# Performance work log

Measured on AMD Instinct MI355X. Metric: run time of the kernel, lower is better.

## Reference

```python
import jax, jax.numpy as jnp
import numpy as np

Q = 10000   # num_question
D = 64      # dim_s
M = 50      # size_m
B = 64      # batch
T = 512     # seq_len


def setup_inputs() -> dict:
    key = jax.random.key(0)
    ks = jax.random.split(key, 14)
    s = 1.0 / np.sqrt(D)
    inp = {
        "question": jax.random.randint(ks[0], (B, T), 0, Q, dtype=jnp.int32),
        "response": jax.random.randint(ks[1], (B, T), 0, 2, dtype=jnp.int32),
        "mask": jnp.ones((B, T), dtype=jnp.float32),
        "k_emb": jax.random.normal(ks[2], (Q, D), jnp.float32) * s,
        "v_emb": jax.random.normal(ks[3], (2 * Q, D), jnp.float32) * s,
        "Mk": jax.random.normal(ks[4], (M, D), jnp.float32) * np.sqrt(2.0 / D),
        "Mv0": jax.random.normal(ks[5], (M, D), jnp.float32) * np.sqrt(2.0 / D),
        "e_W": jax.random.normal(ks[6], (D, D), jnp.float32) * s,
        "e_b": jnp.zeros((D,), jnp.float32),
        "a_W": jax.random.normal(ks[7], (D, D), jnp.float32) * s,
        "a_b": jnp.zeros((D,), jnp.float32),
        "f_W": jax.random.normal(ks[8], (2 * D, D), jnp.float32) * (1.0 / np.sqrt(2 * D)),
        "f_b": jnp.zeros((D,), jnp.float32),
        "p_W": jax.random.normal(ks[9], (D, 1), jnp.float32) * s,
        "p_b": jnp.zeros((1,), jnp.float32),
    }
    return inp


def reference(question, response, mask, k_emb, v_emb, Mk, Mv0,
              e_W, e_b, a_W, a_b, f_W, f_b, p_W, p_b):
    num_q = k_emb.shape[0]
    bsz = question.shape[0]
    x = question + num_q * response                      # [B,T] combined ids
    k = k_emb[question]                                  # [B,T,D]
    v = v_emb[x]                                         # [B,T,D]
    w = jax.nn.softmax(k @ Mk.T, axis=-1)                # [B,T,M] read/write weights
    e = jax.nn.sigmoid(v @ e_W + e_b)                    # [B,T,D] erase
    a = jnp.tanh(v @ a_W + a_b)                          # [B,T,D] add

    def step(Mvt, inp):
        wt, et, at, mt = inp                             # [B,M],[B,D],[B,D],[B]
        Mvn = Mvt * (1.0 - wt[:, :, None] * et[:, None, :]) + wt[:, :, None] * at[:, None, :]
        Mvt = jnp.where(mt[:, None, None] == 1, Mvn, Mvt)
        return Mvt, Mvt

    Mv0b = jnp.broadcast_to(Mv0, (bsz,) + Mv0.shape)     # [B,M,D]
    xs = (jnp.swapaxes(w, 0, 1), jnp.swapaxes(e, 0, 1),
          jnp.swapaxes(a, 0, 1), mask.T)
    _, Mv_seq = jax.lax.scan(step, Mv0b, xs)             # [T,B,M,D] states after steps 0..T-1
    # read at step t (t>=1) uses state after step t-1
    Mv_read = jnp.swapaxes(Mv_seq[:-1], 0, 1)            # [B,T-1,M,D]
    read = jnp.einsum('btm,btmd->btd', w[:, 1:], Mv_read)
    f = jnp.tanh(jnp.concatenate([read, k[:, 1:]], axis=-1) @ f_W + f_b)
    p = (f @ p_W + p_b).squeeze(-1)                      # [B,T-1]
    return p
```

## Files before the change

kernel.cpp:

```cpp
#include <hip/hip_runtime.h>
#include <cstddef>

#define QN 10000
#define DD 64
#define MM 50
#define BB 64
#define TT 512
#define WPAD 52
#define MG 25

__global__ __launch_bounds__(256) void kPre(
    const int* __restrict__ question, const int* __restrict__ response,
    const float* __restrict__ mask,
    const float* __restrict__ k_emb, const float* __restrict__ v_emb,
    const float* __restrict__ Mk,
    const float* __restrict__ e_W, const float* __restrict__ e_b,
    const float* __restrict__ a_W, const float* __restrict__ a_b,
    float* __restrict__ w_buf, float* __restrict__ e_buf,
    float* __restrict__ a_buf) {
  const int lane = (int)(threadIdx.x & 63);
  const int wslot = __builtin_amdgcn_readfirstlane((int)(threadIdx.x >> 6));
  const int gw = blockIdx.x * 4 + wslot;
  const int NW = gridDim.x * 4;
  const int third = NW / 3;
  if (gw >= 3 * third) return;
  const int role = gw / third;
  const int idx = gw - role * third;
  const int stride4 = third * 4;

  if (role == 0) {
    float mk[64];
    const int mrow = lane < MM ? lane : (MM - 1);
#pragma unroll
    for (int i = 0; i < 64; i += 4) {
      const float4 t4 = *(const float4*)(Mk + mrow * 64 + i);
      mk[i] = t4.x; mk[i + 1] = t4.y; mk[i + 2] = t4.z; mk[i + 3] = t4.w;
    }
    for (int base = idx * 4; base < BB * TT; base += stride4) {
      const int4 q4 = *(const int4*)(question + base);
      const float* __restrict__ kr0 = k_emb + (size_t)q4.x * 64;
      const float* __restrict__ kr1 = k_emb + (size_t)q4.y * 64;
      const float* __restrict__ kr2 = k_emb + (size_t)q4.z * 64;
      const float* __restrict__ kr3 = k_emb + (size_t)q4.w * 64;
      float l00=0.f,l01=0.f,l02=0.f,l03=0.f;
      float l10=0.f,l11=0.f,l12=0.f,l13=0.f;
      float l20=0.f,l21=0.f,l22=0.f,l23=0.f;
      float l30=0.f,l31=0.f,l32=0.f,l33=0.f;
#pragma unroll
      for (int i = 0; i < 64; i += 4) {
        const float4 k0 = *(const float4*)(kr0 + i);
        const float4 k1 = *(const float4*)(kr1 + i);
        const float4 k2 = *(const float4*)(kr2 + i);
        const float4 k3 = *(const float4*)(kr3 + i);
        l00 = fmaf(k0.x, mk[i], l00); l01 = fmaf(k0.y, mk[i+1], l01);
        l02 = fmaf(k0.z, mk[i+2], l02); l03 = fmaf(k0.w, mk[i+3], l03);
        l10 = fmaf(k1.x, mk[i], l10); l11 = fmaf(k1.y, mk[i+1], l11);
        l12 = fmaf(k1.z, mk[i+2], l12); l13 = fmaf(k1.w, mk[i+3], l13);
        l20 = fmaf(k2.x, mk[i], l20); l21 = fmaf(k2.y, mk[i+1], l21);
        l22 = fmaf(k2.z, mk[i+2], l22); l23 = fmaf(k2.w, mk[i+3], l23);
        l30 = fmaf(k3.x, mk[i], l30); l31 = fmaf(k3.y, mk[i+1], l31);
        l32 = fmaf(k3.z, mk[i+2], l32); l33 = fmaf(k3.w, mk[i+3], l33);
      }
      float lm[4];
      lm[0] = (l00 + l01) + (l02 + l03);
      lm[1] = (l10 + l11) + (l12 + l13);
      lm[2] = (l20 + l21) + (l22 + l23);
      lm[3] = (l30 + l31) + (l32 + l33);
#pragma unroll
      for (int r = 0; r < 4; ++r) {
        float lv = (lane < MM) ? lm[r] : -3.4e38f;
#pragma unroll
        for (int off = 32; off > 0; off >>= 1) lv = fmaxf(lv, __shfl_xor(lv, off));
        float pe = (lane < MM) ? __expf(lm[r] - lv) : 0.f;
        float ss = pe;
#pragma unroll
        for (int off = 32; off > 0; off >>= 1) ss += __shfl_xor(ss, off);
        if (lane < MM) w_buf[(size_t)(base + r) * WPAD + lane] = pe / ss;
      }
    }
  } else if (role == 1) {
    float ew[64];
#pragma unroll
    for (int i = 0; i < 64; ++i) ew[i] = e_W[i * 64 + lane];
    const float eb = e_b[lane];
    for (int base = idx * 4; base < BB * TT; base += stride4) {
      const int4 q4 = *(const int4*)(question + base);
      const int4 r4 = *(const int4*)(response + base);
      const float4 m4 = *(const float4*)(mask + base);
      const float* __restrict__ v0 = v_emb + ((size_t)q4.x + (size_t)QN * r4.x) * 64;
      const float* __restrict__ v1 = v_emb + ((size_t)q4.y + (size_t)QN * r4.y) * 64;
      const float* __restrict__ v2 = v_emb + ((size_t)q4.z + (size_t)QN * r4.z) * 64;
      const float* __restrict__ v3 = v_emb + ((size_t)q4.w + (size_t)QN * r4.w) * 64;
      float e00 = eb, e01 = 0.f, e10 = eb, e11 = 0.f;
      float e20 = eb, e21 = 0.f, e30 = eb, e31 = 0.f;
#pragma unroll
      for (int i = 0; i < 64; i += 2) {
        const float2 a0 = *(const float2*)(v0 + i);
        const float2 a1 = *(const float2*)(v1 + i);
        const float2 a2 = *(const float2*)(v2 + i);
        const float2 a3 = *(const float2*)(v3 + i);
        e00 = fmaf(a0.x, ew[i], e00); e01 = fmaf(a0.y, ew[i+1], e01);
        e10 = fmaf(a1.x, ew[i], e10); e11 = fmaf(a1.y, ew[i+1], e11);
        e20 = fmaf(a2.x, ew[i], e20); e21 = fmaf(a2.y, ew[i+1], e21);
        e30 = fmaf(a3.x, ew[i], e30); e31 = fmaf(a3.y, ew[i+1], e31);
      }
      const float mf0 = (m4.x == 1.0f) ? 1.0f : 0.0f;
      const float mf1 = (m4.y == 1.0f) ? 1.0f : 0.0f;
      const float mf2 = (m4.z == 1.0f) ? 1.0f : 0.0f;
      const float mf3 = (m4.w == 1.0f) ? 1.0f : 0.0f;
      e_buf[(size_t)(base + 0) * 64 + lane] = mf0 / (1.f + __expf(-(e00 + e01)));
      e_buf[(size_t)(base + 1) * 64 + lane] = mf1 / (1.f + __expf(-(e10 + e11)));
      e_buf[(size_t)(base + 2) * 64 + lane] = mf2 / (1.f + __expf(-(e20 + e21)));
      e_buf[(size_t)(base + 3) * 64 + lane] = mf3 / (1.f + __expf(-(e30 + e31)));
    }
  } else {
    float aw[64];
#pragma unroll
    for (int i = 0; i < 64; ++i) aw[i] = a_W[i * 64 + lane];
    const float ab = a_b[lane];
    for (int base = idx * 4; base < BB * TT; base += stride4) {
      const int4 q4 = *(const int4*)(question + base);
      const int4 r4 = *(const int4*)(response + base);
      const float4 m4 = *(const float4*)(mask + base);
      const float* __restrict__ v0 = v_emb + ((size_t)q4.x + (size_t)QN * r4.x) * 64;
      const float* __restrict__ v1 = v_emb + ((size_t)q4.y + (size_t)QN * r4.y) * 64;
      const float* __restrict__ v2 = v_emb + ((size_t)q4.z + (size_t)QN * r4.z) * 64;
      const float* __restrict__ v3 = v_emb + ((size_t)q4.w + (size_t)QN * r4.w) * 64;
      float a00 = ab, a01 = 0.f, a10 = ab, a11 = 0.f;
      float a20 = ab, a21 = 0.f, a30 = ab, a31 = 0.f;
#pragma unroll
      for (int i = 0; i < 64; i += 2) {
        const float2 x0 = *(const float2*)(v0 + i);
        const float2 x1 = *(const float2*)(v1 + i);
        const float2 x2 = *(const float2*)(v2 + i);
        const float2 x3 = *(const float2*)(v3 + i);
        a00 = fmaf(x0.x, aw[i], a00); a01 = fmaf(x0.y, aw[i+1], a01);
        a10 = fmaf(x1.x, aw[i], a10); a11 = fmaf(x1.y, aw[i+1], a11);
        a20 = fmaf(x2.x, aw[i], a20); a21 = fmaf(x2.y, aw[i+1], a21);
        a30 = fmaf(x3.x, aw[i], a30); a31 = fmaf(x3.y, aw[i+1], a31);
      }
      const float mf0 = (m4.x == 1.0f) ? 1.0f : 0.0f;
      const float mf1 = (m4.y == 1.0f) ? 1.0f : 0.0f;
      const float mf2 = (m4.z == 1.0f) ? 1.0f : 0.0f;
      const float mf3 = (m4.w == 1.0f) ? 1.0f : 0.0f;
      const float s0 = a00 + a01, s1 = a10 + a11, s2 = a20 + a21, s3 = a30 + a31;
      a_buf[(size_t)(base + 0) * 64 + lane] = mf0 * (1.f - 2.f / (__expf(2.f * s0) + 1.f));
      a_buf[(size_t)(base + 1) * 64 + lane] = mf1 * (1.f - 2.f / (__expf(2.f * s1) + 1.f));
      a_buf[(size_t)(base + 2) * 64 + lane] = mf2 * (1.f - 2.f / (__expf(2.f * s2) + 1.f));
      a_buf[(size_t)(base + 3) * 64 + lane] = mf3 * (1.f - 2.f / (__expf(2.f * s3) + 1.f));
    }
  }
}

__global__ __launch_bounds__(256) void kA16(
    const float* __restrict__ w_buf, const float* __restrict__ e_buf,
    const float* __restrict__ a_buf, float* __restrict__ AB) {
  const int lane = (int)(threadIdx.x & 63);
  const int wslot = __builtin_amdgcn_readfirstlane((int)(threadIdx.x >> 6));
  const int u2 = blockIdx.x * 4 + wslot;
  if (u2 >= BB * 32 * 2) return;
  const int g = u2 & 1;
  const int unit = u2 >> 1;
  const int b = unit >> 5;
  const int c = unit & 31;
  const size_t rowbase = (size_t)b * TT + c * 16;
  const size_t eb0 = rowbase * 64 + lane;

  float ev[16], av[16];
#pragma unroll
  for (int j = 0; j < 16; ++j) {
    ev[j] = e_buf[eb0 + (size_t)j * 64];
    av[j] = a_buf[eb0 + (size_t)j * 64];
  }

  float Am[MG], Bm[MG];
#pragma unroll
  for (int m = 0; m < MG; ++m) { Am[m] = 1.f; Bm[m] = 0.f; }

#pragma unroll
  for (int j = 0; j < 16; ++j) {
    const float* __restrict__ wr = w_buf + (rowbase + j) * WPAD + g * MG;
#pragma unroll
    for (int m = 0; m < MG; ++m) {
      const float wm = wr[m];
      const float al = fmaf(-wm, ev[j], 1.0f);
      const float be = wm * av[j];
      Am[m] *= al;
      Bm[m] = fmaf(Bm[m], al, be);
    }
  }
  float* __restrict__ abp = AB + (size_t)unit * 6400 + (g * MG) * 128 + lane * 2;
#pragma unroll
  for (int m = 0; m < MG; ++m) {
    float2 o; o.x = Am[m]; o.y = Bm[m];
    *(float2*)(abp + m * 128) = o;
  }
}

__global__ __launch_bounds__(256) void kB_entry(
    const float* __restrict__ AB, const float* __restrict__ Mv0,
    float* __restrict__ entry, int C) {
  const int NT = gridDim.x * 256;
  for (int idx = blockIdx.x * 256 + (int)threadIdx.x; idx < BB * MM * 64;
       idx += NT) {
    const int b = idx / (MM * 64);
    const int r = idx - b * (MM * 64);
    float s = Mv0[r];
    const float* __restrict__ abp = AB + (size_t)b * C * 6400 + (size_t)r * 2;
    float* __restrict__ ep = entry + (size_t)b * C * 3200 + r;
    if (C == 32) {
      float2 ab[32];
#pragma unroll
      for (int c = 0; c < 32; ++c)
        ab[c] = *(const float2*)(abp + (size_t)c * 6400);
#pragma unroll
      for (int c = 0; c < 32; ++c) {
        ep[(size_t)c * 3200] = s;
        s = fmaf(ab[c].x, s, ab[c].y);
      }
    } else {
      float2 cur = *(const float2*)(abp);
      for (int c = 0; c < C; ++c) {
        ep[(size_t)c * 3200] = s;
        float2 nxt; nxt.x = 1.f; nxt.y = 0.f;
        if (c + 1 < C) nxt = *(const float2*)(abp + (size_t)(c + 1) * 6400);
        s = fmaf(cur.x, s, cur.y);
        cur = nxt;
      }
    }
  }
}

__global__ __launch_bounds__(256) void kC16(
    const float* __restrict__ w_buf, const float* __restrict__ e_buf,
    const float* __restrict__ a_buf, const float* __restrict__ entry,
    float* __restrict__ read2) {
  const int lane = (int)(threadIdx.x & 63);
  const int wslot = __builtin_amdgcn_readfirstlane((int)(threadIdx.x >> 6));
  const int u2 = blockIdx.x * 4 + wslot;
  if (u2 >= BB * 32 * 2) return;
  const int g = u2 & 1;
  const int unit = u2 >> 1;
  const int b = unit >> 5;
  const int c = unit & 31;
  const size_t RN = (size_t)BB * (TT - 1) * 64;
  const size_t rowbase = (size_t)b * TT + c * 16;
  const size_t eb0 = rowbase * 64 + lane;

  float ev[16], av[16];
#pragma unroll
  for (int j = 0; j < 16; ++j) {
    ev[j] = e_buf[eb0 + (size_t)j * 64];
    av[j] = a_buf[eb0 + (size_t)j * 64];
  }

  float s[MG];
  {
    const float* __restrict__ ep =
        entry + (size_t)unit * 3200 + (g * MG) * 64 + lane;
#pragma unroll
    for (int m = 0; m < MG; ++m) s[m] = ep[m * 64];
  }

  const int t0 = c * 16;
  float* __restrict__ rb = read2 + (size_t)g * RN;
#pragma unroll
  for (int j = 0; j < 16; ++j) {
    const int t = t0 + j;
    const float* __restrict__ wr = w_buf + (rowbase + j) * WPAD + g * MG;
    if (t >= 1) {
      float a0 = 0.f, a1 = 0.f;
#pragma unroll
      for (int m = 0; m < MG - 1; m += 2) {
        a0 = fmaf(wr[m], s[m], a0);
        a1 = fmaf(wr[m + 1], s[m + 1], a1);
      }
      a0 = fmaf(wr[MG - 1], s[MG - 1], a0);
      rb[((size_t)b * (TT - 1) + (t - 1)) * 64 + lane] = a0 + a1;
    }
#pragma unroll
    for (int m = 0; m < MG; ++m)
      s[m] = fmaf(wr[m], fmaf(-s[m], ev[j], av[j]), s[m]);
  }
}

__global__ __launch_bounds__(256) void kA_chunk(
    const float* __restrict__ w_buf, const float* __restrict__ e_buf,
    const float* __restrict__ a_buf, float* __restrict__ AB, int logC, int L) {
  const int lane = (int)(threadIdx.x & 63);
  const int wslot = __builtin_amdgcn_readfirstlane((int)(threadIdx.x >> 6));
  const int NW = gridDim.x * 4;
  const int C = 1 << logC;
  for (int u2 = blockIdx.x * 4 + wslot; u2 < BB * C * 2; u2 += NW) {
    const int g = u2 & 1;
    const int unit = u2 >> 1;
    const int b = unit >> logC;
    const int c = unit & (C - 1);
    float Am[MG], Bm[MG];
#pragma unroll
    for (int m = 0; m < MG; ++m) { Am[m] = 1.f; Bm[m] = 0.f; }
    const size_t rowbase = (size_t)b * TT + c * L;
#pragma unroll 2
    for (int j = 0; j < L; ++j) {
      const size_t row = rowbase + j;
      const float ed = e_buf[row * 64 + lane];
      const float ad = a_buf[row * 64 + lane];
      const float* __restrict__ wr = w_buf + row * WPAD + g * MG;
#pragma unroll
      for (int m = 0; m < MG; ++m) {
        const float wm = wr[m];
        const float al = fmaf(-wm, ed, 1.0f);
        const float be = wm * ad;
        Am[m] *= al;
        Bm[m] = fmaf(Bm[m], al, be);
      }
    }
    float* __restrict__ abp = AB + (size_t)unit * 6400 + (g * MG) * 128 + lane * 2;
#pragma unroll
    for (int m = 0; m < MG; ++m) {
      float2 o; o.x = Am[m]; o.y = Bm[m];
      *(float2*)(abp + m * 128) = o;
    }
  }
}

__global__ __launch_bounds__(256) void kC_read(
    const float* __restrict__ w_buf, const float* __restrict__ e_buf,
    const float* __restrict__ a_buf, const float* __restrict__ entry,
    const float* __restrict__ Mv0, float* __restrict__ read2,
    int logC, int L, int use_mv0) {
  const int lane = (int)(threadIdx.x & 63);
  const int wslot = __builtin_amdgcn_readfirstlane((int)(threadIdx.x >> 6));
  const int NW = gridDim.x * 4;
  const int C = 1 << logC;
  const size_t RN = (size_t)BB * (TT - 1) * 64;
  for (int u2 = blockIdx.x * 4 + wslot; u2 < BB * C * 2; u2 += NW) {
    const int g = u2 & 1;
    const int unit = u2 >> 1;
    const int b = unit >> logC;
    const int c = unit & (C - 1);
    float s[MG];
    if (use_mv0) {
#pragma unroll
      for (int m = 0; m < MG; ++m) s[m] = Mv0[(g * MG + m) * 64 + lane];
    } else {
      const float* __restrict__ ep =
          entry + (size_t)unit * 3200 + (g * MG) * 64 + lane;
#pragma unroll
      for (int m = 0; m < MG; ++m) s[m] = ep[m * 64];
    }
    const int t0 = c * L;
    float* __restrict__ rb = read2 + (size_t)g * RN;
    for (int j = 0; j < L; ++j) {
      const int t = t0 + j;
      const size_t row = (size_t)b * TT + t;
      const float ed = e_buf[row * 64 + lane];
      const float ad = a_buf[row * 64 + lane];
      const float* __restrict__ wr = w_buf + row * WPAD + g * MG;
      if (t >= 1) {
        float a0 = 0.f, a1 = 0.f;
#pragma unroll
        for (int m = 0; m < MG - 1; m += 2) {
          a0 = fmaf(wr[m], s[m], a0);
          a1 = fmaf(wr[m + 1], s[m + 1], a1);
        }
        a0 = fmaf(wr[MG - 1], s[MG - 1], a0);
        rb[((size_t)b * (TT - 1) + (t - 1)) * 64 + lane] = a0 + a1;
      }
#pragma unroll
      for (int m = 0; m < MG; ++m)
        s[m] = fmaf(wr[m], fmaf(-s[m], ed, ad), s[m]);
    }
  }
}

__global__ __launch_bounds__(256) void k3_out(
    const int* __restrict__ question, const float* __restrict__ k_emb,
    const float* __restrict__ read2,
    const float* __restrict__ f_W, const float* __restrict__ f_b,
    const float* __restrict__ p_W, const float* __restrict__ p_b,
    float* __restrict__ out) {
  const int lane = (int)(threadIdx.x & 63);
  const int wslot = __builtin_amdgcn_readfirstlane((int)(threadIdx.x >> 6));
  const int NW = gridDim.x * 4;
  const size_t RN = (size_t)BB * (TT - 1) * 64;

  float fw[128];
#pragma unroll
  for (int i = 0; i < 128; ++i) fw[i] = f_W[i * 64 + lane];
  const float fb = f_b[lane];
  const float pw = p_W[lane];
  const float pb = p_b[0];

  for (int row = blockIdx.x * 4 + wslot; row < BB * (TT - 1); row += NW) {
    const int b = row / (TT - 1);
    const int tp = row - b * (TT - 1);
    const float* __restrict__ r0 = read2 + (size_t)row * 64;
    const float* __restrict__ r1 = r0 + RN;
    const int qn = question[b * TT + tp + 1];
    const float* __restrict__ krow = k_emb + (size_t)qn * 64;

    float f0 = fb, f1 = 0.f, f2 = 0.f, f3 = 0.f;
#pragma unroll
    for (int i = 0; i < 64; i += 4) {
      const float4 x0 = *(const float4*)(r0 + i);
      const float4 x1 = *(const float4*)(r1 + i);
      f0 = fmaf(x0.x + x1.x, fw[i], f0);
      f1 = fmaf(x0.y + x1.y, fw[i + 1], f1);
      f2 = fmaf(x0.z + x1.z, fw[i + 2], f2);
      f3 = fmaf(x0.w + x1.w, fw[i + 3], f3);
    }
#pragma unroll
    for (int i = 0; i < 64; i += 4) {
      const float4 kv = *(const float4*)(krow + i);
      f0 = fmaf(kv.x, fw[64 + i], f0);
      f1 = fmaf(kv.y, fw[64 + i + 1], f1);
      f2 = fmaf(kv.z, fw[64 + i + 2], f2);
      f3 = fmaf(kv.w, fw[64 + i + 3], f3);
    }
    const float f = (f0 + f1) + (f2 + f3);
    const float t2 = __expf(2.f * f);
    const float fv = 1.f - 2.f / (t2 + 1.f);
    float acc = fv * pw;
#pragma unroll
    for (int off = 32; off > 0; off >>= 1) acc += __shfl_xor(acc, off);
    if (lane == 0) out[row] = acc + pb;
  }
}

extern "C" void kernel_launch(void* const* d_in, const int* in_sizes, int n_in,
                              void* d_out, int out_size, void* d_ws, size_t ws_size,
                              hipStream_t stream) {
  const int*   question = (const int*)d_in[0];
  const int*   response = (const int*)d_in[1];
  const float* mask     = (const float*)d_in[2];
  const float* k_emb    = (const float*)d_in[3];
  const float* v_emb    = (const float*)d_in[4];
  const float* Mk       = (const float*)d_in[5];
  const float* Mv0      = (const float*)d_in[6];
  const float* e_W      = (const float*)d_in[7];
  const float* e_b      = (const float*)d_in[8];
  const float* a_W      = (const float*)d_in[9];
  const float* a_b      = (const float*)d_in[10];
  const float* f_W      = (const float*)d_in[11];
  const float* f_b      = (const float*)d_in[12];
  const float* p_W      = (const float*)d_in[13];
  const float* p_b      = (const float*)d_in[14];
  float* out = (float*)d_out;

  const size_t wN  = (size_t)BB * TT * WPAD;
  const size_t eN  = (size_t)BB * TT * 64;
  const size_t r2N = 2ull * BB * (TT - 1) * 64;
  float* ws = (float*)d_ws;
  float* w_buf  = ws;
  float* e_buf  = w_buf + wN;
  float* a_buf  = e_buf + eN;
  float* read2  = a_buf + eN;
  float* AB_arr = read2 + r2N;
  const size_t baseN = wN + 2 * eN + r2N;

  int C = 32, logC = 5;
  while (C >= 2) {
    const size_t need = (baseN + 9600ull * BB * C) * sizeof(float);
    if (need <= ws_size) break;
    C >>= 1; logC -= 1;
  }
  int useChunks = (C >= 2);
  if (!useChunks) { C = 1; logC = 0; }
  const int L = TT / C;
  float* entry = AB_arr + 6400ull * BB * C;

  hipLaunchKernelGGL(kPre, dim3(2048), dim3(256), 0, stream,
                     question, response, mask, k_emb, v_emb, Mk,
                     e_W, e_b, a_W, a_b, w_buf, e_buf, a_buf);

  if (C == 32) {
    hipLaunchKernelGGL(kA16, dim3(1024), dim3(256), 0, stream,
                       w_buf, e_buf, a_buf, AB_arr);
    hipLaunchKernelGGL(kB_entry, dim3((BB * MM * 64 + 255) / 256), dim3(256),
                       0, stream, AB_arr, Mv0, entry, C);
    hipLaunchKernelGGL(kC16, dim3(1024), dim3(256), 0, stream,
                       w_buf, e_buf, a_buf, entry, read2);
  } else {
    if (useChunks) {
      const int ublocksA = (BB * C * 2 + 3) / 4;
      hipLaunchKernelGGL(kA_chunk, dim3(ublocksA), dim3(256), 0, stream,
                         w_buf, e_buf, a_buf, AB_arr, logC, L);
      hipLaunchKernelGGL(kB_entry, dim3((BB * MM * 64 + 255) / 256), dim3(256),
                         0, stream, AB_arr, Mv0, entry, C);
    }
    const int ublocksC = (BB * C * 2 + 3) / 4;
    hipLaunchKernelGGL(kC_read, dim3(ublocksC), dim3(256), 0, stream,
                       w_buf, e_buf, a_buf, entry, Mv0, read2,
                       logC, L, useChunks ? 0 : 1);
  }

  hipLaunchKernelGGL(k3_out, dim3(1024), dim3(256), 0, stream,
                     question, k_emb, read2, f_W, f_b, p_W, p_b, out);
}
```

Baseline: 211.4 us.

## Stage gathered embedding rows through LDS and prefetch next row in output kernel

In the precompute and output kernels, each lane now loads one element of each gathered embedding or read row with a coalesced load and writes it to a per-wave LDS buffer. The dot products then read broadcast float4 values from LDS instead of every lane issuing redundant wide global loads of the same row. The output kernel also software-prefetches the next row's read and key data. Empty asm constraints pin the weight arrays in VGPRs to stop the compiler rematerializing them. The LDS round trip relies on wave-synchronous execution with no barrier, and the pinning raises register pressure.

After: 225.6 us. +6.7%, slower.

```diff
diff --git a/kernel.cpp b/kernel.cpp
--- a/kernel.cpp
+++ b/kernel.cpp
@@ -8,6 +8,10 @@
 #define TT 512
 #define WPAD 52
 #define MG 25
+
+#define PIN(arr, n)                                        \
+  _Pragma("unroll") for (int _p = 0; _p < (n); ++_p)       \
+      asm volatile("" : "+v"((arr)[_p]));
 
 __global__ __launch_bounds__(256) void kPre(
     const int* __restrict__ question, const int* __restrict__ response,
@@ -18,9 +22,10 @@
     const float* __restrict__ a_W, const float* __restrict__ a_b,
     float* __restrict__ w_buf, float* __restrict__ e_buf,
     float* __restrict__ a_buf) {
+  __shared__ float stg[4][4][64];
   const int lane = (int)(threadIdx.x & 63);
-  const int wslot = __builtin_amdgcn_readfirstlane((int)(threadIdx.x >> 6));
-  const int gw = blockIdx.x * 4 + wslot;
+  const int ws = __builtin_amdgcn_readfirstlane((int)(threadIdx.x >> 6));
+  const int gw = blockIdx.x * 4 + ws;
   const int NW = gridDim.x * 4;
   const int third = NW / 3;
   if (gw >= 3 * third) return;
@@ -36,36 +41,31 @@
       const float4 t4 = *(const float4*)(Mk + mrow * 64 + i);
       mk[i] = t4.x; mk[i + 1] = t4.y; mk[i + 2] = t4.z; mk[i + 3] = t4.w;
     }
+    PIN(mk, 64)
     for (int base = idx * 4; base < BB * TT; base += stride4) {
       const int4 q4 = *(const int4*)(question + base);
-      const float* __restrict__ kr0 = k_emb + (size_t)q4.x * 64;
-      const float* __restrict__ kr1 = k_emb + (size_t)q4.y * 64;
-      const float* __restrict__ kr2 = k_emb + (size_t)q4.z * 64;
-      const float* __restrict__ kr3 = k_emb + (size_t)q4.w * 64;
-      float l00=0.f,l01=0.f,l02=0.f,l03=0.f;
-      float l10=0.f,l11=0.f,l12=0.f,l13=0.f;
-      float l20=0.f,l21=0.f,l22=0.f,l23=0.f;
-      float l30=0.f,l31=0.f,l32=0.f,l33=0.f;
-#pragma unroll
-      for (int i = 0; i < 64; i += 4) {
-        const float4 k0 = *(const float4*)(kr0 + i);
-        const float4 k1 = *(const float4*)(kr1 + i);
-        const float4 k2 = *(const float4*)(kr2 + i);
-        const float4 k3 = *(const float4*)(kr3 + i);
-        l00 = fmaf(k0.x, mk[i], l00); l01 = fmaf(k0.y, mk[i+1], l01);
-        l02 = fmaf(k0.z, mk[i+2], l02); l03 = fmaf(k0.w, mk[i+3], l03);
-        l10 = fmaf(k1.x, mk[i], l10); l11 = fmaf(k1.y, mk[i+1], l11);
-        l12 = fmaf(k1.z, mk[i+2], l12); l13 = fmaf(k1.w, mk[i+3], l13);
-        l20 = fmaf(k2.x, mk[i], l20); l21 = fmaf(k2.y, mk[i+1], l21);
-        l22 = fmaf(k2.z, mk[i+2], l22); l23 = fmaf(k2.w, mk[i+3], l23);
-        l30 = fmaf(k3.x, mk[i], l30); l31 = fmaf(k3.y, mk[i+1], l31);
-        l32 = fmaf(k3.z, mk[i+2], l32); l33 = fmaf(k3.w, mk[i+3], l33);
-      }
+      const float kl0 = k_emb[(size_t)q4.x * 64 + lane];
+      const float kl1 = k_emb[(size_t)q4.y * 64 + lane];
+      const float kl2 = k_emb[(size_t)q4.z * 64 + lane];
+      const float kl3 = k_emb[(size_t)q4.w * 64 + lane];
+      stg[ws][0][lane] = kl0;
+      stg[ws][1][lane] = kl1;
+      stg[ws][2][lane] = kl2;
+      stg[ws][3][lane] = kl3;
       float lm[4];
-      lm[0] = (l00 + l01) + (l02 + l03);
-      lm[1] = (l10 + l11) + (l12 + l13);
-      lm[2] = (l20 + l21) + (l22 + l23);
-      lm[3] = (l30 + l31) + (l32 + l33);
+#pragma unroll
+      for (int r = 0; r < 4; ++r) {
+        float l0 = 0.f, l1 = 0.f, l2 = 0.f, l3 = 0.f;
+#pragma unroll
+        for (int i = 0; i < 64; i += 4) {
+          const float4 kv = *(const float4*)&stg[ws][r][i];
+          l0 = fmaf(kv.x, mk[i], l0);
+          l1 = fmaf(kv.y, mk[i + 1], l1);
+          l2 = fmaf(kv.z, mk[i + 2], l2);
+          l3 = fmaf(kv.w, mk[i + 3], l3);
+        }
+        lm[r] = (l0 + l1) + (l2 + l3);
+      }
 #pragma unroll
       for (int r = 0; r < 4; ++r) {
         float lv = (lane < MM) ? lm[r] : -3.4e38f;
@@ -82,27 +82,36 @@
     float ew[64];
 #pragma unroll
     for (int i = 0; i < 64; ++i) ew[i] = e_W[i * 64 + lane];
+    PIN(ew, 64)
     const float eb = e_b[lane];
     for (int base = idx * 4; base < BB * TT; base += stride4) {
       const int4 q4 = *(const int4*)(question + base);
       const int4 r4 = *(const int4*)(response + base);
       const float4 m4 = *(const float4*)(mask + base);
-      const float* __restrict__ v0 = v_emb + ((size_t)q4.x + (size_t)QN * r4.x) * 64;
-      const float* __restrict__ v1 = v_emb + ((size_t)q4.y + (size_t)QN * r4.y) * 64;
-      const float* __restrict__ v2 = v_emb + ((size_t)q4.z + (size_t)QN * r4.z) * 64;
-      const float* __restrict__ v3 = v_emb + ((size_t)q4.w + (size_t)QN * r4.w) * 64;
+      const float vl0 = v_emb[((size_t)q4.x + (size_t)QN * r4.x) * 64 + lane];
+      const float vl1 = v_emb[((size_t)q4.y + (size_t)QN * r4.y) * 64 + lane];
+      const float vl2 = v_emb[((size_t)q4.z + (size_t)QN * r4.z) * 64 + lane];
+      const float vl3 = v_emb[((size_t)q4.w + (size_t)QN * r4.w) * 64 + lane];
+      stg[ws][0][lane] = vl0;
+      stg[ws][1][lane] = vl1;
+      stg[ws][2][lane] = vl2;
+      stg[ws][3][lane] = vl3;
       float e00 = eb, e01 = 0.f, e10 = eb, e11 = 0.f;
       float e20 = eb, e21 = 0.f, e30 = eb, e31 = 0.f;
 #pragma unroll
-      for (int i = 0; i < 64; i += 2) {
-        const float2 a0 = *(const float2*)(v0 + i);
-        const float2 a1 = *(const float2*)(v1 + i);
-        const float2 a2 = *(const float2*)(v2 + i);
-        const float2 a3 = *(const float2*)(v3 + i);
-        e00 = fmaf(a0.x, ew[i], e00); e01 = fmaf(a0.y, ew[i+1], e01);
-        e10 = fmaf(a1.x, ew[i], e10); e11 = fmaf(a1.y, ew[i+1], e11);
-        e20 = fmaf(a2.x, ew[i], e20); e21 = fmaf(a2.y, ew[i+1], e21);
-        e30 = fmaf(a3.x, ew[i], e30); e31 = fmaf(a3.y, ew[i+1], e31);
+      for (int i = 0; i < 64; i += 4) {
+        const float4 v0 = *(const float4*)&stg[ws][0][i];
+        const float4 v1 = *(const float4*)&stg[ws][1][i];
+        const float4 v2 = *(const float4*)&stg[ws][2][i];
+        const float4 v3 = *(const float4*)&stg[ws][3][i];
+        e00 = fmaf(v0.x, ew[i], e00);     e01 = fmaf(v0.y, ew[i + 1], e01);
+        e00 = fmaf(v0.z, ew[i + 2], e00); e01 = fmaf(v0.w, ew[i + 3], e01);
+        e10 = fmaf(v1.x, ew[i], e10);     e11 = fmaf(v1.y, ew[i + 1], e11);
+        e10 = fmaf(v1.z, ew[i + 2], e10); e11 = fmaf(v1.w, ew[i + 3], e11);
+        e20 = fmaf(v2.x, ew[i], e20);     e21 = fmaf(v2.y, ew[i + 1], e21);
+        e20 = fmaf(v2.z, ew[i + 2], e20); e21 = fmaf(v2.w, ew[i + 3], e21);
+        e30 = fmaf(v3.x, ew[i], e30);     e31 = fmaf(v3.y, ew[i + 1], e31);
+        e30 = fmaf(v3.z, ew[i + 2], e30); e31 = fmaf(v3.w, ew[i + 3], e31);
       }
       const float mf0 = (m4.x == 1.0f) ? 1.0f : 0.0f;
       const float mf1 = (m4.y == 1.0f) ? 1.0f : 0.0f;
@@ -117,27 +126,36 @@
     float aw[64];
 #pragma unroll
     for (int i = 0; i < 64; ++i) aw[i] = a_W[i * 64 + lane];
+    PIN(aw, 64)
     const float ab = a_b[lane];
     for (int base = idx * 4; base < BB * TT; base += stride4) {
       const int4 q4 = *(const int4*)(question + base);
       const int4 r4 = *(const int4*)(response + base);
       const float4 m4 = *(const float4*)(mask + base);
-      const float* __restrict__ v0 = v_emb + ((size_t)q4.x + (size_t)QN * r4.x) * 64;
-      const float* __restrict__ v1 = v_emb + ((size_t)q4.y + (size_t)QN * r4.y) * 64;
-      const float* __restrict__ v2 = v_emb + ((size_t)q4.z + (size_t)QN * r4.z) * 64;
-      const float* __restrict__ v3 = v_emb + ((size_t)q4.w + (size_t)QN * r4.w) * 64;
+      const float vl0 = v_emb[((size_t)q4.x + (size_t)QN * r4.x) * 64 + lane];
+      const float vl1 = v_emb[((size_t)q4.y + (size_t)QN * r4.y) * 64 + lane];
+      const float vl2 = v_emb[((size_t)q4.z + (size_t)QN * r4.z) * 64 + lane];
+      const float vl3 = v_emb[((size_t)q4.w + (size_t)QN * r4.w) * 64 + lane];
+      stg[ws][0][lane] = vl0;
+      stg[ws][1][lane] = vl1;
+      stg[ws][2][lane] = vl2;
+      stg[ws][3][lane] = vl3;
       float a00 = ab, a01 = 0.f, a10 = ab, a11 = 0.f;
       float a20 = ab, a21 = 0.f, a30 = ab, a31 = 0.f;
 #pragma unroll
-      for (int i = 0; i < 64; i += 2) {
-        const float2 x0 = *(const float2*)(v0 + i);
-        const float2 x1 = *(const float2*)(v1 + i);
-        const float2 x2 = *(const float2*)(v2 + i);
-        const float2 x3 = *(const float2*)(v3 + i);
-        a00 = fmaf(x0.x, aw[i], a00); a01 = fmaf(x0.y, aw[i+1], a01);
-        a10 = fmaf(x1.x, aw[i], a10); a11 = fmaf(x1.y, aw[i+1], a11);
-        a20 = fmaf(x2.x, aw[i], a20); a21 = fmaf(x2.y, aw[i+1], a21);
-        a30 = fmaf(x3.x, aw[i], a30); a31 = fmaf(x3.y, aw[i+1], a31);
+      for (int i = 0; i < 64; i += 4) {
+        const float4 v0 = *(const float4*)&stg[ws][0][i];
+        const float4 v1 = *(const float4*)&stg[ws][1][i];
+        const float4 v2 = *(const float4*)&stg[ws][2][i];
+        const float4 v3 = *(const float4*)&stg[ws][3][i];
+        a00 = fmaf(v0.x, aw[i], a00);     a01 = fmaf(v0.y, aw[i + 1], a01);
+        a00 = fmaf(v0.z, aw[i + 2], a00); a01 = fmaf(v0.w, aw[i + 3], a01);
+        a10 = fmaf(v1.x, aw[i], a10);     a11 = fmaf(v1.y, aw[i + 1], a11);
+        a10 = fmaf(v1.z, aw[i + 2], a10); a11 = fmaf(v1.w, aw[i + 3], a11);
+        a20 = fmaf(v2.x, aw[i], a20);     a21 = fmaf(v2.y, aw[i + 1], a21);
+        a20 = fmaf(v2.z, aw[i + 2], a20); a21 = fmaf(v2.w, aw[i + 3], a21);
+        a30 = fmaf(v3.x, aw[i], a30);     a31 = fmaf(v3.y, aw[i + 1], a31);
+        a30 = fmaf(v3.z, aw[i + 2], a30); a31 = fmaf(v3.w, aw[i + 3], a31);
       }
       const float mf0 = (m4.x == 1.0f) ? 1.0f : 0.0f;
       const float mf1 = (m4.y == 1.0f) ? 1.0f : 0.0f;
@@ -380,39 +398,55 @@
     const float* __restrict__ f_W, const float* __restrict__ f_b,
     const float* __restrict__ p_W, const float* __restrict__ p_b,
     float* __restrict__ out) {
+  __shared__ float stg[4][2][64];
   const int lane = (int)(threadIdx.x & 63);
-  const int wslot = __builtin_amdgcn_readfirstlane((int)(threadIdx.x >> 6));
+  const int ws = __builtin_amdgcn_readfirstlane((int)(threadIdx.x >> 6));
   const int NW = gridDim.x * 4;
   const size_t RN = (size_t)BB * (TT - 1) * 64;
+  const int R = BB * (TT - 1);
 
   float fw[128];
 #pragma unroll
   for (int i = 0; i < 128; ++i) fw[i] = f_W[i * 64 + lane];
+  PIN(fw, 128)
   const float fb = f_b[lane];
   const float pw = p_W[lane];
   const float pb = p_b[0];
 
-  for (int row = blockIdx.x * 4 + wslot; row < BB * (TT - 1); row += NW) {
+  int row = blockIdx.x * 4 + ws;
+  float rd = 0.f, kl = 0.f;
+  if (row < R) {
+    rd = read2[(size_t)row * 64 + lane] + read2[RN + (size_t)row * 64 + lane];
     const int b = row / (TT - 1);
     const int tp = row - b * (TT - 1);
-    const float* __restrict__ r0 = read2 + (size_t)row * 64;
-    const float* __restrict__ r1 = r0 + RN;
     const int qn = question[b * TT + tp + 1];
-    const float* __restrict__ krow = k_emb + (size_t)qn * 64;
-
+    kl = k_emb[(size_t)qn * 64 + lane];
+  }
+  while (row < R) {
+    const int nrow = row + NW;
+    float nrd = 0.f, nkl = 0.f;
+    if (nrow < R) {
+      nrd = read2[(size_t)nrow * 64 + lane] +
+            read2[RN + (size_t)nrow * 64 + lane];
+      const int nb = nrow / (TT - 1);
+      const int ntp = nrow - nb * (TT - 1);
+      const int nqn = question[nb * TT + ntp + 1];
+      nkl = k_emb[(size_t)nqn * 64 + lane];
+    }
+    stg[ws][0][lane] = rd;
+    stg[ws][1][lane] = kl;
     float f0 = fb, f1 = 0.f, f2 = 0.f, f3 = 0.f;
 #pragma unroll
     for (int i = 0; i < 64; i += 4) {
-      const float4 x0 = *(const float4*)(r0 + i);
-      const float4 x1 = *(const float4*)(r1 + i);
-      f0 = fmaf(x0.x + x1.x, fw[i], f0);
-      f1 = fmaf(x0.y + x1.y, fw[i + 1], f1);
-      f2 = fmaf(x0.z + x1.z, fw[i + 2], f2);
-      f3 = fmaf(x0.w + x1.w, fw[i + 3], f3);
+      const float4 xv = *(const float4*)&stg[ws][0][i];
+      f0 = fmaf(xv.x, fw[i], f0);
+      f1 = fmaf(xv.y, fw[i + 1], f1);
+      f2 = fmaf(xv.z, fw[i + 2], f2);
+      f3 = fmaf(xv.w, fw[i + 3], f3);
     }
 #pragma unroll
     for (int i = 0; i < 64; i += 4) {
-      const float4 kv = *(const float4*)(krow + i);
+      const float4 kv = *(const float4*)&stg[ws][1][i];
       f0 = fmaf(kv.x, fw[64 + i], f0);
       f1 = fmaf(kv.y, fw[64 + i + 1], f1);
       f2 = fmaf(kv.z, fw[64 + i + 2], f2);
@@ -425,6 +459,8 @@
 #pragma unroll
     for (int off = 32; off > 0; off >>= 1) acc += __shfl_xor(acc, off);
     if (lane == 0) out[row] = acc + pb;
+
+    rd = nrd; kl = nkl; row = nrow;
   }
 }
 
```

## Replace chunked parallel scan with single-pass per-batch sequential scan kernel

Applied to the files above, without the earlier changes.

Drops the three-phase chunked scan (chunk transfer coefficients, entry-state propagation, re-scan with reads). In its place is one kernel per batch row: four compute waves each own a slice of the memory rows, producer waves double-buffer e/a/w into LDS, and a writer wave reduces the partial reads into a single read buffer. This removes the AB and entry intermediate traffic, two kernel launches and the duplicated scan work. The cost is a fully serial 512-step loop on only 64 blocks, which leaves most of the GPU idle and adds a block barrier every chunk. The output kernel is also changed to prefetch the next row, stage it through LDS and pin the weight registers.

Result: slower. 310.7 us (+46.9%).

```diff
diff --git a/kernel.cpp b/kernel.cpp
--- a/kernel.cpp
+++ b/kernel.cpp
@@ -7,7 +7,10 @@
 #define BB 64
 #define TT 512
 #define WPAD 52
-#define MG 25
+
+#define PIN(arr, n)                                        \
+  _Pragma("unroll") for (int _p = 0; _p < (n); ++_p)       \
+      asm volatile("" : "+v"((arr)[_p]));
 
 __global__ __launch_bounds__(256) void kPre(
     const int* __restrict__ question, const int* __restrict__ response,
@@ -152,267 +155,181 @@
   }
 }
 
-__global__ __launch_bounds__(256) void kA16(
+__global__ __launch_bounds__(512) void kScan(
     const float* __restrict__ w_buf, const float* __restrict__ e_buf,
-    const float* __restrict__ a_buf, float* __restrict__ AB) {
+    const float* __restrict__ a_buf, const float* __restrict__ Mv0,
+    float* __restrict__ read_buf) {
+  __shared__ float e_lds[2][16][64];
+  __shared__ float a_lds[2][16][64];
+  __shared__ float w_lds[2][4][16][16];
+  __shared__ float p_lds[2][4][16][64];
   const int lane = (int)(threadIdx.x & 63);
-  const int wslot = __builtin_amdgcn_readfirstlane((int)(threadIdx.x >> 6));
-  const int u2 = blockIdx.x * 4 + wslot;
-  if (u2 >= BB * 32 * 2) return;
-  const int g = u2 & 1;
-  const int unit = u2 >> 1;
-  const int b = unit >> 5;
-  const int c = unit & 31;
-  const size_t rowbase = (size_t)b * TT + c * 16;
-  const size_t eb0 = rowbase * 64 + lane;
-
-  float ev[16], av[16];
-#pragma unroll
-  for (int j = 0; j < 16; ++j) {
-    ev[j] = e_buf[eb0 + (size_t)j * 64];
-    av[j] = a_buf[eb0 + (size_t)j * 64];
-  }
-
-  float Am[MG], Bm[MG];
-#pragma unroll
-  for (int m = 0; m < MG; ++m) { Am[m] = 1.f; Bm[m] = 0.f; }
-
-#pragma unroll
-  for (int j = 0; j < 16; ++j) {
-    const float* __restrict__ wr = w_buf + (rowbase + j) * WPAD + g * MG;
-#pragma unroll
-    for (int m = 0; m < MG; ++m) {
-      const float wm = wr[m];
-      const float al = fmaf(-wm, ev[j], 1.0f);
-      const float be = wm * av[j];
-      Am[m] *= al;
-      Bm[m] = fmaf(Bm[m], al, be);
-    }
-  }
-  float* __restrict__ abp = AB + (size_t)unit * 6400 + (g * MG) * 128 + lane * 2;
-#pragma unroll
-  for (int m = 0; m < MG; ++m) {
-    float2 o; o.x = Am[m]; o.y = Bm[m];
-    *(float2*)(abp + m * 128) = o;
-  }
-}
-
-__global__ __launch_bounds__(256) void kB_entry(
-    const float* __restrict__ AB, const float* __restrict__ Mv0,
-    float* __restrict__ entry, int C) {
-  const int NT = gridDim.x * 256;
-  for (int idx = blockIdx.x * 256 + (int)threadIdx.x; idx < BB * MM * 64;
-       idx += NT) {
-    const int b = idx / (MM * 64);
-    const int r = idx - b * (MM * 64);
-    float s = Mv0[r];
-    const float* __restrict__ abp = AB + (size_t)b * C * 6400 + (size_t)r * 2;
-    float* __restrict__ ep = entry + (size_t)b * C * 3200 + r;
-    if (C == 32) {
-      float2 ab[32];
-#pragma unroll
-      for (int c = 0; c < 32; ++c)
-        ab[c] = *(const float2*)(abp + (size_t)c * 6400);
-#pragma unroll
-      for (int c = 0; c < 32; ++c) {
-        ep[(size_t)c * 3200] = s;
-        s = fmaf(ab[c].x, s, ab[c].y);
+  const int ws = __builtin_amdgcn_readfirstlane((int)(threadIdx.x >> 6));
+  const int b = blockIdx.x;
+  const size_t bbase = (size_t)b * TT;
+
+  float s[13];
+  if (ws < 4) {
+    const int gbase = (ws < 2) ? ws * 13 : 26 + (ws - 2) * 12;
+    const int gcnt  = (ws < 2) ? 13 : 12;
+#pragma unroll
+    for (int m = 0; m < 13; ++m)
+      s[m] = (m < gcnt) ? Mv0[(gbase + m) * 64 + lane] : 0.f;
+  }
+
+  if (ws == 4) {
+#pragma unroll
+    for (int j = 0; j < 16; ++j)
+      e_lds[0][j][lane] = e_buf[(bbase + j) * 64 + lane];
+  } else if (ws == 5) {
+#pragma unroll
+    for (int j = 0; j < 16; ++j)
+      a_lds[0][j][lane] = a_buf[(bbase + j) * 64 + lane];
+  } else if (ws == 6) {
+#pragma unroll
+    for (int j = 0; j < 16; ++j) {
+      if (lane < MM) {
+        const float v = w_buf[(bbase + j) * WPAD + lane];
+        const int grp = (lane < 13) ? 0 : (lane < 26) ? 1 : (lane < 38) ? 2 : 3;
+        const int gb = (grp < 2) ? grp * 13 : 26 + (grp - 2) * 12;
+        w_lds[0][grp][j][lane - gb] = v;
+      } else if (lane == 50) w_lds[0][2][j][12] = 0.f;
+      else if (lane == 51) w_lds[0][3][j][12] = 0.f;
+    }
+  }
+  __syncthreads();
+
+  for (int c = 0; c < 32; ++c) {
+    const int p = c & 1;
+    if (ws < 4) {
+      const int g = ws;
+#pragma unroll
+      for (int j = 0; j < 16; ++j) {
+        const float4 q0 = *(const float4*)&w_lds[p][g][j][0];
+        const float4 q1 = *(const float4*)&w_lds[p][g][j][4];
+        const float4 q2 = *(const float4*)&w_lds[p][g][j][8];
+        const float4 q3 = *(const float4*)&w_lds[p][g][j][12];
+        const float ed = e_lds[p][j][lane];
+        const float ad = a_lds[p][j][lane];
+        const float wm[13] = {q0.x, q0.y, q0.z, q0.w, q1.x, q1.y, q1.z, q1.w,
+                              q2.x, q2.y, q2.z, q2.w, q3.x};
+        float d0 = 0.f, d1 = 0.f;
+#pragma unroll
+        for (int m = 0; m < 12; m += 2) {
+          d0 = fmaf(wm[m], s[m], d0);
+          d1 = fmaf(wm[m + 1], s[m + 1], d1);
+        }
+        d0 = fmaf(wm[12], s[12], d0);
+        p_lds[p][g][j][lane] = d0 + d1;
+#pragma unroll
+        for (int m = 0; m < 13; ++m)
+          s[m] = fmaf(wm[m], fmaf(-s[m], ed, ad), s[m]);
+      }
+    } else if (ws == 4) {
+      if (c + 1 < 32) {
+        const size_t rb = bbase + (size_t)(c + 1) * 16;
+#pragma unroll
+        for (int j = 0; j < 16; ++j)
+          e_lds[1 - p][j][lane] = e_buf[(rb + j) * 64 + lane];
+      }
+    } else if (ws == 5) {
+      if (c + 1 < 32) {
+        const size_t rb = bbase + (size_t)(c + 1) * 16;
+#pragma unroll
+        for (int j = 0; j < 16; ++j)
+          a_lds[1 - p][j][lane] = a_buf[(rb + j) * 64 + lane];
+      }
+    } else if (ws == 6) {
+      if (c + 1 < 32) {
+        const size_t rb = bbase + (size_t)(c + 1) * 16;
+#pragma unroll
+        for (int j = 0; j < 16; ++j) {
+          if (lane < MM) {
+            const float v = w_buf[(rb + j) * WPAD + lane];
+            const int grp = (lane < 13) ? 0 : (lane < 26) ? 1 : (lane < 38) ? 2 : 3;
+            const int gb = (grp < 2) ? grp * 13 : 26 + (grp - 2) * 12;
+            w_lds[1 - p][grp][j][lane - gb] = v;
+          } else if (lane == 50) w_lds[1 - p][2][j][12] = 0.f;
+          else if (lane == 51) w_lds[1 - p][3][j][12] = 0.f;
+        }
       }
     } else {
-      float2 cur = *(const float2*)(abp);
-      for (int c = 0; c < C; ++c) {
-        ep[(size_t)c * 3200] = s;
-        float2 nxt; nxt.x = 1.f; nxt.y = 0.f;
-        if (c + 1 < C) nxt = *(const float2*)(abp + (size_t)(c + 1) * 6400);
-        s = fmaf(cur.x, s, cur.y);
-        cur = nxt;
-      }
-    }
-  }
-}
-
-__global__ __launch_bounds__(256) void kC16(
-    const float* __restrict__ w_buf, const float* __restrict__ e_buf,
-    const float* __restrict__ a_buf, const float* __restrict__ entry,
-    float* __restrict__ read2) {
-  const int lane = (int)(threadIdx.x & 63);
-  const int wslot = __builtin_amdgcn_readfirstlane((int)(threadIdx.x >> 6));
-  const int u2 = blockIdx.x * 4 + wslot;
-  if (u2 >= BB * 32 * 2) return;
-  const int g = u2 & 1;
-  const int unit = u2 >> 1;
-  const int b = unit >> 5;
-  const int c = unit & 31;
-  const size_t RN = (size_t)BB * (TT - 1) * 64;
-  const size_t rowbase = (size_t)b * TT + c * 16;
-  const size_t eb0 = rowbase * 64 + lane;
-
-  float ev[16], av[16];
-#pragma unroll
-  for (int j = 0; j < 16; ++j) {
-    ev[j] = e_buf[eb0 + (size_t)j * 64];
-    av[j] = a_buf[eb0 + (size_t)j * 64];
-  }
-
-  float s[MG];
-  {
-    const float* __restrict__ ep =
-        entry + (size_t)unit * 3200 + (g * MG) * 64 + lane;
-#pragma unroll
-    for (int m = 0; m < MG; ++m) s[m] = ep[m * 64];
-  }
-
-  const int t0 = c * 16;
-  float* __restrict__ rb = read2 + (size_t)g * RN;
-#pragma unroll
-  for (int j = 0; j < 16; ++j) {
-    const int t = t0 + j;
-    const float* __restrict__ wr = w_buf + (rowbase + j) * WPAD + g * MG;
-    if (t >= 1) {
-      float a0 = 0.f, a1 = 0.f;
-#pragma unroll
-      for (int m = 0; m < MG - 1; m += 2) {
-        a0 = fmaf(wr[m], s[m], a0);
-        a1 = fmaf(wr[m + 1], s[m + 1], a1);
-      }
-      a0 = fmaf(wr[MG - 1], s[MG - 1], a0);
-      rb[((size_t)b * (TT - 1) + (t - 1)) * 64 + lane] = a0 + a1;
-    }
-#pragma unroll
-    for (int m = 0; m < MG; ++m)
-      s[m] = fmaf(wr[m], fmaf(-s[m], ev[j], av[j]), s[m]);
-  }
-}
-
-__global__ __launch_bounds__(256) void kA_chunk(
-    const float* __restrict__ w_buf, const float* __restrict__ e_buf,
-    const float* __restrict__ a_buf, float* __restrict__ AB, int logC, int L) {
-  const int lane = (int)(threadIdx.x & 63);
-  const int wslot = __builtin_amdgcn_readfirstlane((int)(threadIdx.x >> 6));
-  const int NW = gridDim.x * 4;
-  const int C = 1 << logC;
-  for (int u2 = blockIdx.x * 4 + wslot; u2 < BB * C * 2; u2 += NW) {
-    const int g = u2 & 1;
-    const int unit = u2 >> 1;
-    const int b = unit >> logC;
-    const int c = unit & (C - 1);
-    float Am[MG], Bm[MG];
-#pragma unroll
-    for (int m = 0; m < MG; ++m) { Am[m] = 1.f; Bm[m] = 0.f; }
-    const size_t rowbase = (size_t)b * TT + c * L;
-#pragma unroll 2
-    for (int j = 0; j < L; ++j) {
-      const size_t row = rowbase + j;
-      const float ed = e_buf[row * 64 + lane];
-      const float ad = a_buf[row * 64 + lane];
-      const float* __restrict__ wr = w_buf + row * WPAD + g * MG;
-#pragma unroll
-      for (int m = 0; m < MG; ++m) {
-        const float wm = wr[m];
-        const float al = fmaf(-wm, ed, 1.0f);
-        const float be = wm * ad;
-        Am[m] *= al;
-        Bm[m] = fmaf(Bm[m], al, be);
-      }
-    }
-    float* __restrict__ abp = AB + (size_t)unit * 6400 + (g * MG) * 128 + lane * 2;
-#pragma unroll
-    for (int m = 0; m < MG; ++m) {
-      float2 o; o.x = Am[m]; o.y = Bm[m];
-      *(float2*)(abp + m * 128) = o;
-    }
-  }
-}
-
-__global__ __launch_bounds__(256) void kC_read(
-    const float* __restrict__ w_buf, const float* __restrict__ e_buf,
-    const float* __restrict__ a_buf, const float* __restrict__ entry,
-    const float* __restrict__ Mv0, float* __restrict__ read2,
-    int logC, int L, int use_mv0) {
-  const int lane = (int)(threadIdx.x & 63);
-  const int wslot = __builtin_amdgcn_readfirstlane((int)(threadIdx.x >> 6));
-  const int NW = gridDim.x * 4;
-  const int C = 1 << logC;
-  const size_t RN = (size_t)BB * (TT - 1) * 64;
-  for (int u2 = blockIdx.x * 4 + wslot; u2 < BB * C * 2; u2 += NW) {
-    const int g = u2 & 1;
-    const int unit = u2 >> 1;
-    const int b = unit >> logC;
-    const int c = unit & (C - 1);
-    float s[MG];
-    if (use_mv0) {
-#pragma unroll
-      for (int m = 0; m < MG; ++m) s[m] = Mv0[(g * MG + m) * 64 + lane];
-    } else {
-      const float* __restrict__ ep =
-          entry + (size_t)unit * 3200 + (g * MG) * 64 + lane;
-#pragma unroll
-      for (int m = 0; m < MG; ++m) s[m] = ep[m * 64];
-    }
-    const int t0 = c * L;
-    float* __restrict__ rb = read2 + (size_t)g * RN;
-    for (int j = 0; j < L; ++j) {
-      const int t = t0 + j;
-      const size_t row = (size_t)b * TT + t;
-      const float ed = e_buf[row * 64 + lane];
-      const float ad = a_buf[row * 64 + lane];
-      const float* __restrict__ wr = w_buf + row * WPAD + g * MG;
-      if (t >= 1) {
-        float a0 = 0.f, a1 = 0.f;
-#pragma unroll
-        for (int m = 0; m < MG - 1; m += 2) {
-          a0 = fmaf(wr[m], s[m], a0);
-          a1 = fmaf(wr[m + 1], s[m + 1], a1);
+      if (c >= 1) {
+        const int cc = c - 1, q = 1 - p;
+        const int j0 = (cc == 0) ? 1 : 0;
+        for (int j = j0; j < 16; ++j) {
+          const int t = cc * 16 + j;
+          const float r = (p_lds[q][0][j][lane] + p_lds[q][1][j][lane]) +
+                          (p_lds[q][2][j][lane] + p_lds[q][3][j][lane]);
+          read_buf[((size_t)b * (TT - 1) + (t - 1)) * 64 + lane] = r;
         }
-        a0 = fmaf(wr[MG - 1], s[MG - 1], a0);
-        rb[((size_t)b * (TT - 1) + (t - 1)) * 64 + lane] = a0 + a1;
-      }
-#pragma unroll
-      for (int m = 0; m < MG; ++m)
-        s[m] = fmaf(wr[m], fmaf(-s[m], ed, ad), s[m]);
+      }
+    }
+    __syncthreads();
+  }
+  if (ws == 7) {
+    for (int j = 0; j < 16; ++j) {
+      const int t = 31 * 16 + j;
+      const float r = (p_lds[1][0][j][lane] + p_lds[1][1][j][lane]) +
+                      (p_lds[1][2][j][lane] + p_lds[1][3][j][lane]);
+      read_buf[((size_t)b * (TT - 1) + (t - 1)) * 64 + lane] = r;
     }
   }
 }
 
 __global__ __launch_bounds__(256) void k3_out(
     const int* __restrict__ question, const float* __restrict__ k_emb,
-    const float* __restrict__ read2,
+    const float* __restrict__ read_buf,
     const float* __restrict__ f_W, const float* __restrict__ f_b,
     const float* __restrict__ p_W, const float* __restrict__ p_b,
     float* __restrict__ out) {
+  __shared__ float stg[4][2][64];
   const int lane = (int)(threadIdx.x & 63);
-  const int wslot = __builtin_amdgcn_readfirstlane((int)(threadIdx.x >> 6));
+  const int ws = __builtin_amdgcn_readfirstlane((int)(threadIdx.x >> 6));
   const int NW = gridDim.x * 4;
-  const size_t RN = (size_t)BB * (TT - 1) * 64;
+  const int R = BB * (TT - 1);
 
   float fw[128];
 #pragma unroll
   for (int i = 0; i < 128; ++i) fw[i] = f_W[i * 64 + lane];
+  PIN(fw, 128)
   const float fb = f_b[lane];
   const float pw = p_W[lane];
   const float pb = p_b[0];
 
-  for (int row = blockIdx.x * 4 + wslot; row < BB * (TT - 1); row += NW) {
+  int row = blockIdx.x * 4 + ws;
+  float rd = 0.f, kl = 0.f;
+  if (row < R) {
+    rd = read_buf[(size_t)row * 64 + lane];
     const int b = row / (TT - 1);
     const int tp = row - b * (TT - 1);
-    const float* __restrict__ r0 = read2 + (size_t)row * 64;
-    const float* __restrict__ r1 = r0 + RN;
     const int qn = question[b * TT + tp + 1];
-    const float* __restrict__ krow = k_emb + (size_t)qn * 64;
-
+    kl = k_emb[(size_t)qn * 64 + lane];
+  }
+  while (row < R) {
+    const int nrow = row + NW;
+    float nrd = 0.f, nkl = 0.f;
+    if (nrow < R) {
+      nrd = read_buf[(size_t)nrow * 64 + lane];
+      const int nb = nrow / (TT - 1);
+      const int ntp = nrow - nb * (TT - 1);
+      const int nqn = question[nb * TT + ntp + 1];
+      nkl = k_emb[(size_t)nqn * 64 + lane];
+    }
+    stg[ws][0][lane] = rd;
+    stg[ws][1][lane] = kl;
     float f0 = fb, f1 = 0.f, f2 = 0.f, f3 = 0.f;
 #pragma unroll
     for (int i = 0; i < 64; i += 4) {
-      const float4 x0 = *(const float4*)(r0 + i);
-      const float4 x1 = *(const float4*)(r1 + i);
-      f0 = fmaf(x0.x + x1.x, fw[i], f0);
-      f1 = fmaf(x0.y + x1.y, fw[i + 1], f1);
-      f2 = fmaf(x0.z + x1.z, fw[i + 2], f2);
-      f3 = fmaf(x0.w + x1.w, fw[i + 3], f3);
+      const float4 xv = *(const float4*)&stg[ws][0][i];
+      f0 = fmaf(xv.x, fw[i], f0);
+      f1 = fmaf(xv.y, fw[i + 1], f1);
+      f2 = fmaf(xv.z, fw[i + 2], f2);
+      f3 = fmaf(xv.w, fw[i + 3], f3);
     }
 #pragma unroll
     for (int i = 0; i < 64; i += 4) {
-      const float4 kv = *(const float4*)(krow + i);
+      const float4 kv = *(const float4*)&stg[ws][1][i];
       f0 = fmaf(kv.x, fw[64 + i], f0);
       f1 = fmaf(kv.y, fw[64 + i + 1], f1);
       f2 = fmaf(kv.z, fw[64 + i + 2], f2);
@@ -425,6 +342,8 @@
 #pragma unroll
     for (int off = 32; off > 0; off >>= 1) acc += __shfl_xor(acc, off);
     if (lane == 0) out[row] = acc + pb;
+
+    rd = nrd; kl = nkl; row = nrow;
   }
 }
 
@@ -450,51 +369,17 @@
 
   const size_t wN  = (size_t)BB * TT * WPAD;
   const size_t eN  = (size_t)BB * TT * 64;
-  const size_t r2N = 2ull * BB * (TT - 1) * 64;
   float* ws = (float*)d_ws;
-  float* w_buf  = ws;
-  float* e_buf  = w_buf + wN;
-  float* a_buf  = e_buf + eN;
-  float* read2  = a_buf + eN;
-  float* AB_arr = read2 + r2N;
-  const size_t baseN = wN + 2 * eN + r2N;
-
-  int C = 32, logC = 5;
-  while (C >= 2) {
-    const size_t need = (baseN + 9600ull * BB * C) * sizeof(float);
-    if (need <= ws_size) break;
-    C >>= 1; logC -= 1;
-  }
-  int useChunks = (C >= 2);
-  if (!useChunks) { C = 1; logC = 0; }
-  const int L = TT / C;
-  float* entry = AB_arr + 6400ull * BB * C;
+  float* w_buf    = ws;
+  float* e_buf    = w_buf + wN;
+  float* a_buf    = e_buf + eN;
+  float* read_buf = a_buf + eN;
 
   hipLaunchKernelGGL(kPre, dim3(2048), dim3(256), 0, stream,
                      question, response, mask, k_emb, v_emb, Mk,
                      e_W, e_b, a_W, a_b, w_buf, e_buf, a_buf);
-
-  if (C == 32) {
-    hipLaunchKernelGGL(kA16, dim3(1024), dim3(256), 0, stream,
-                       w_buf, e_buf, a_buf, AB_arr);
-    hipLaunchKernelGGL(kB_entry, dim3((BB * MM * 64 + 255) / 256), dim3(256),
-                       0, stream, AB_arr, Mv0, entry, C);
-    hipLaunchKernelGGL(kC16, dim3(1024), dim3(256), 0, stream,
-                       w_buf, e_buf, a_buf, entry, read2);
-  } else {
-    if (useChunks) {
-      const int ublocksA = (BB * C * 2 + 3) / 4;
-      hipLaunchKernelGGL(kA_chunk, dim3(ublocksA), dim3(256), 0, stream,
-                         w_buf, e_buf, a_buf, AB_arr, logC, L);
-      hipLaunchKernelGGL(kB_entry, dim3((BB * MM * 64 + 255) / 256), dim3(256),
-                         0, stream, AB_arr, Mv0, entry, C);
-    }
-    const int ublocksC = (BB * C * 2 + 3) / 4;
-    hipLaunchKernelGGL(kC_read, dim3(ublocksC), dim3(256), 0, stream,
-                       w_buf, e_buf, a_buf, entry, Mv0, read2,
-                       logC, L, useChunks ? 0 : 1);
-  }
-
+  hipLaunchKernelGGL(kScan, dim3(BB), dim3(512), 0, stream,
+                     w_buf, e_buf, a_buf, Mv0, read_buf);
   hipLaunchKernelGGL(k3_out, dim3(1024), dim3(256), 0, stream,
-                     question, k_emb, read2, f_W, f_b, p_W, p_b, out);
+                     question, k_emb, read_buf, f_W, f_b, p_W, p_b, out);
 }
```
